# Kernel tuning notes

Hardware: AMD Instinct MI355X
Metric: run time of the kernel (lower is better)

## Reference

```python
import jax, jax.numpy as jnp
import numpy as np
import math

N_HEAD = 16
ROPE_BASE = 10000.0


def _rope(xh):
    # xh: [B, H, T, D]; rotate full head dim using half-split (GPT-NeoX style)
    B, H, T, D = xh.shape
    theta = 1.0 / (ROPE_BASE ** (jnp.arange(0, D, 2, dtype=jnp.float32) / D))  # [D/2]
    idx_theta = jnp.arange(T, dtype=jnp.float32)[:, None] * theta[None, :]      # [T, D/2]
    idx_theta2 = jnp.concatenate([idx_theta, idx_theta], axis=1)                 # [T, D]
    cos = jnp.cos(idx_theta2)[None, None]                                        # [1,1,T,D]
    sin = jnp.sin(idx_theta2)[None, None]
    d2 = D // 2
    neg_half = jnp.concatenate([-xh[..., d2:], xh[..., :d2]], axis=-1)
    return xh * cos + neg_half * sin


def setup_inputs() -> dict:
    key = jax.random.key(0)
    k1, k2, k3 = jax.random.split(key, 3)
    B, T, C = 2, 2048, 2048
    x = jax.random.normal(k1, (B, T, C), dtype=jnp.float32)
    w_attn = jax.random.normal(k2, (C, 3 * C), dtype=jnp.float32) * (1.0 / math.sqrt(C))
    w_proj = jax.random.normal(k3, (C, C), dtype=jnp.float32) * (1.0 / math.sqrt(C))
    return {"x": x, "w_attn": w_attn, "w_proj": w_proj}


def reference(x, w_attn, w_proj):
    B, T, C = x.shape
    H = N_HEAD
    D = C // H
    qkv = x @ w_attn                                   # [B,T,3C]
    q, k, v = jnp.split(qkv, 3, axis=-1)
    # [B,T,C] -> [B,H,T,D]
    to_heads = lambda t: t.reshape(B, T, H, D).transpose(0, 2, 1, 3)
    q, k, v = to_heads(q), to_heads(k), to_heads(v)
    q = _rope(q)
    k = _rope(k)
    att = jnp.einsum('bhqd,bhkd->bhqk', q, k) * (1.0 / math.sqrt(D))
    causal = jnp.tril(jnp.ones((T, T), dtype=bool))
    att = jnp.where(causal[None, None], att, -jnp.inf)
    att = jax.nn.softmax(att, axis=-1)
    y = jnp.einsum('bhqk,bhkd->bhqd', att, v)          # [B,H,T,D]
    y = y.transpose(0, 2, 1, 3).reshape(B, T, C)
    return y @ w_proj
```

## Files before the change

kernel.cpp:

```cpp
#include <hip/hip_runtime.h>
#include <hip/hip_bf16.h>
#include <math.h>

typedef __bf16 bf16;
typedef __bf16 bf16x8 __attribute__((ext_vector_type(8)));
typedef float f32x4 __attribute__((ext_vector_type(4)));
typedef float f32x16 __attribute__((ext_vector_type(16)));
typedef unsigned int u32x2 __attribute__((ext_vector_type(2)));
typedef unsigned int u32x4 __attribute__((ext_vector_type(4)));

#define MFMA16(a, b, c) __builtin_amdgcn_mfma_f32_16x16x32_bf16((a), (b), (c), 0, 0, 0)
#define MFMA32(a, b, c) __builtin_amdgcn_mfma_f32_32x32x16_bf16((a), (b), (c), 0, 0, 0)

static constexpr int Bsz = 2, Tsz = 2048, Csz = 2048, Hn = 16, Dh = 128;
static constexpr float ATTN_SCALE = 0.08838834764831845f;

__device__ __forceinline__ void gld16(const void* src, void* dst) {
    __builtin_amdgcn_global_load_lds((__attribute__((address_space(1))) void*)src,
                                     (__attribute__((address_space(3))) void*)dst,
                                     16, 0, 0);
}

__device__ __forceinline__ unsigned cvt_pk_bf16(float lo, float hi) {
    unsigned r;
    asm("v_cvt_pk_bf16_f32 %0, %1, %2" : "=v"(r) : "v"(lo), "v"(hi));
    return r;
}

__device__ __forceinline__ bf16x8 make_pfrag(float p0, float p1, float p2, float p3,
                                             float p4, float p5, float p6, float p7) {
    unsigned a0 = cvt_pk_bf16(p0, p1), a1 = cvt_pk_bf16(p2, p3);
    unsigned b0 = cvt_pk_bf16(p4, p5), b1 = cvt_pk_bf16(p6, p7);
    asm volatile("v_permlane32_swap_b32 %0, %1" : "+v"(a0), "+v"(b0));
    asm volatile("v_permlane32_swap_b32 %0, %1" : "+v"(a1), "+v"(b1));
    u32x4 w = {a0, a1, b0, b1};
    return __builtin_bit_cast(bf16x8, w);
}

__global__ __launch_bounds__(256) void cast_x_kernel(const float* __restrict__ x,
                                                     bf16* __restrict__ o, int n8) {
    int i = blockIdx.x * 256 + threadIdx.x;
    if (i >= n8) return;
    const float4* x4 = (const float4*)x;
    float4 a = x4[2 * i], b = x4[2 * i + 1];
    bf16x8 v;
    v[0] = (bf16)a.x; v[1] = (bf16)a.y; v[2] = (bf16)a.z; v[3] = (bf16)a.w;
    v[4] = (bf16)b.x; v[5] = (bf16)b.y; v[6] = (bf16)b.z; v[7] = (bf16)b.w;
    ((bf16x8*)o)[i] = v;
}

template <typename TIN>
__global__ __launch_bounds__(256) void transpose_cast_kernel(const TIN* __restrict__ in,
                                                             bf16* __restrict__ out,
                                                             int R, int Cc) {
    __shared__ float tile[64][65];
    const int tx = threadIdx.x, ty = threadIdx.y;
    in  += (size_t)blockIdx.z * R * Cc;
    out += (size_t)blockIdx.z * R * Cc;
    const int c0 = blockIdx.x * 64, r0 = blockIdx.y * 64;
#pragma unroll
    for (int j = 0; j < 16; ++j) {
        int rr = ty + j * 4;
        tile[rr][tx] = (float)in[(size_t)(r0 + rr) * Cc + c0 + tx];
    }
    __syncthreads();
#pragma unroll
    for (int j = 0; j < 16; ++j) {
        int cc = ty + j * 4;
        out[(size_t)(c0 + cc) * R + r0 + tx] = (bf16)tile[tx][cc];
    }
}

__global__ __launch_bounds__(256) void cossin_kernel(float2* __restrict__ cs) {
    int idx = blockIdx.x * 256 + threadIdx.x;
    int t = idx >> 6, i = idx & 63;
    float theta = 1.0f / powf(10000.0f, (float)(2 * i) / 128.0f);
    float ang = (float)t * theta;
    cs[idx] = make_float2(cosf(ang), sinf(ang));
}

__global__ __launch_bounds__(512, 2)
void gemm384_qkv(const bf16* __restrict__ A, const bf16* __restrict__ Bt,
                 bf16* __restrict__ Oq, bf16* __restrict__ Ok, bf16* __restrict__ Ov,
                 const float2* __restrict__ cs, int K) {
    __shared__ bf16 sA[2][128 * 64];
    __shared__ bf16 sB[2][384 * 64];
    const int tid = threadIdx.x, lane = tid & 63, wid = tid >> 6;
    const int wm = wid >> 2, wn = wid & 3;
    const int lo16 = lane & 15, hi4 = lane >> 4;

    const int cpx = gridDim.x >> 3;
    const int swz = (blockIdx.x & 7) * cpx + (blockIdx.x >> 3);
    const int by = swz & 31;
    const int bx = swz >> 5;
    const int row0 = by << 7, col0 = bx * 384;

    const int srow = tid >> 3;
    const int swzoff = (((tid & 7) ^ ((tid >> 3) & 7)) << 3);
    const bf16* srcA = A  + (size_t)(row0 + srow) * K + swzoff;
    const bf16* srcB = Bt + (size_t)(col0 + srow) * K + swzoff;
    const size_t K64 = (size_t)K * 64;
    char* const ldsA = (char*)&sA[0][0];
    char* const ldsB = (char*)&sB[0][0];
    const int wuo = wid << 10;

    auto issueA = [&](int c, int kt) {
        const bf16* s = srcA + (size_t)kt * 64;
        gld16(s,       ldsA + c * 16384 + 0    + wuo);
        gld16(s + K64, ldsA + c * 16384 + 8192 + wuo);
    };
    auto issueB = [&](int c, int kt, int u) {
        const bf16* s = srcB + (size_t)kt * 64 + (size_t)(2 * u) * K64;
        gld16(s,       ldsB + c * 49152 + u * 16384 + 0    + wuo);
        gld16(s + K64, ldsB + c * 49152 + u * 16384 + 8192 + wuo);
    };
    auto ldF = [&](const char* buf, int row, int ks) {
        return *(const bf16x8*)(buf + row * 128 + ((((ks << 2) + hi4) ^ (row & 7)) << 4));
    };

    const int arow = (wm << 6) + lo16;
    const int brow = (wn << 4) + lo16;

    f32x4 acc[4][6] = {};
    const int nkt = K >> 6;

    issueA(0, 0); issueB(0, 0, 0); issueB(0, 0, 1); issueB(0, 0, 2);
    asm volatile("s_waitcnt vmcnt(4)" ::: "memory");
    __builtin_amdgcn_s_barrier();

    for (int kt = 0; kt < nkt - 1; ++kt) {
        const int c = kt & 1;
        const char* bufA = ldsA + c * 16384;
        const char* bufB = ldsB + c * 49152;
        bf16x8 af[4][2], bq[2][2];
#pragma unroll
        for (int i = 0; i < 4; ++i) {
            af[i][0] = ldF(bufA, arow + (i << 4), 0);
            af[i][1] = ldF(bufA, arow + (i << 4), 1);
        }
#pragma unroll
        for (int j = 0; j < 2; ++j) {
            bq[j][0] = ldF(bufB, brow + (j << 6), 0);
            bq[j][1] = ldF(bufB, brow + (j << 6), 1);
        }
        issueA(c ^ 1, kt + 1); issueB(c ^ 1, kt + 1, 0); issueB(c ^ 1, kt + 1, 1);
        __builtin_amdgcn_s_barrier();
        asm volatile("s_waitcnt lgkmcnt(0)" ::: "memory");
        __builtin_amdgcn_sched_barrier(0);
        __builtin_amdgcn_s_setprio(1);
#pragma unroll
        for (int ks = 0; ks < 2; ++ks)
#pragma unroll
            for (int i = 0; i < 4; ++i)
#pragma unroll
                for (int j = 0; j < 2; ++j)
                    acc[i][j] = MFMA16(af[i][ks], bq[j][ks], acc[i][j]);
        __builtin_amdgcn_s_setprio(0);
        asm volatile("s_waitcnt vmcnt(8)" ::: "memory");
        __builtin_amdgcn_s_barrier();
#pragma unroll
        for (int j = 0; j < 2; ++j) {
            bq[j][0] = ldF(bufB, brow + ((j + 2) << 6), 0);
            bq[j][1] = ldF(bufB, brow + ((j + 2) << 6), 1);
        }
        issueB(c ^ 1, kt + 1, 2);
        __builtin_amdgcn_s_barrier();
        asm volatile("s_waitcnt lgkmcnt(0)" ::: "memory");
        __builtin_amdgcn_sched_barrier(0);
        __builtin_amdgcn_s_setprio(1);
#pragma unroll
        for (int ks = 0; ks < 2; ++ks)
#pragma unroll
            for (int i = 0; i < 4; ++i)
#pragma unroll
                for (int j = 0; j < 2; ++j)
                    acc[i][j + 2] = MFMA16(af[i][ks], bq[j][ks], acc[i][j + 2]);
        __builtin_amdgcn_s_setprio(0);
        asm volatile("s_waitcnt vmcnt(8)" ::: "memory");
        __builtin_amdgcn_s_barrier();
#pragma unroll
        for (int j = 0; j < 2; ++j) {
            bq[j][0] = ldF(bufB, brow + ((j + 4) << 6), 0);
            bq[j][1] = ldF(bufB, brow + ((j + 4) << 6), 1);
        }
        __builtin_amdgcn_s_barrier();
        asm volatile("s_waitcnt lgkmcnt(0)" ::: "memory");
        __builtin_amdgcn_sched_barrier(0);
        __builtin_amdgcn_s_setprio(1);
#pragma unroll
        for (int ks = 0; ks < 2; ++ks)
#pragma unroll
            for (int i = 0; i < 4; ++i)
#pragma unroll
                for (int j = 0; j < 2; ++j)
                    acc[i][j + 4] = MFMA16(af[i][ks], bq[j][ks], acc[i][j + 4]);
        __builtin_amdgcn_s_setprio(0);
        asm volatile("s_waitcnt vmcnt(4)" ::: "memory");
        __builtin_amdgcn_s_barrier();
    }

    {
        const int c = (nkt - 1) & 1;
        const char* bufA = ldsA + c * 16384;
        const char* bufB = ldsB + c * 49152;
        bf16x8 af[4][2], bq[2][2];
#pragma unroll
        for (int i = 0; i < 4; ++i) {
            af[i][0] = ldF(bufA, arow + (i << 4), 0);
            af[i][1] = ldF(bufA, arow + (i << 4), 1);
        }
#pragma unroll
        for (int j = 0; j < 2; ++j) {
            bq[j][0] = ldF(bufB, brow + (j << 6), 0);
            bq[j][1] = ldF(bufB, brow + (j << 6), 1);
        }
        __builtin_amdgcn_s_barrier();
        asm volatile("s_waitcnt lgkmcnt(0)" ::: "memory");
        __builtin_amdgcn_sched_barrier(0);
        __builtin_amdgcn_s_setprio(1);
#pragma unroll
        for (int ks = 0; ks < 2; ++ks)
#pragma unroll
            for (int i = 0; i < 4; ++i)
#pragma unroll
                for (int j = 0; j < 2; ++j)
                    acc[i][j] = MFMA16(af[i][ks], bq[j][ks], acc[i][j]);
        __builtin_amdgcn_s_setprio(0);
        asm volatile("s_waitcnt vmcnt(2)" ::: "memory");
        __builtin_amdgcn_s_barrier();
#pragma unroll
        for (int j = 0; j < 2; ++j) {
            bq[j][0] = ldF(bufB, brow + ((j + 2) << 6), 0);
            bq[j][1] = ldF(bufB, brow + ((j + 2) << 6), 1);
        }
        __builtin_amdgcn_s_barrier();
        asm volatile("s_waitcnt lgkmcnt(0)" ::: "memory");
        __builtin_amdgcn_sched_barrier(0);
        __builtin_amdgcn_s_setprio(1);
#pragma unroll
        for (int ks = 0; ks < 2; ++ks)
#pragma unroll
            for (int i = 0; i < 4; ++i)
#pragma unroll
                for (int j = 0; j < 2; ++j)
                    acc[i][j + 2] = MFMA16(af[i][ks], bq[j][ks], acc[i][j + 2]);
        __builtin_amdgcn_s_setprio(0);
        asm volatile("s_waitcnt vmcnt(0)" ::: "memory");
        __builtin_amdgcn_s_barrier();
#pragma unroll
        for (int j = 0; j < 2; ++j) {
            bq[j][0] = ldF(bufB, brow + ((j + 4) << 6), 0);
            bq[j][1] = ldF(bufB, brow + ((j + 4) << 6), 1);
        }
        __builtin_amdgcn_s_barrier();
        asm volatile("s_waitcnt lgkmcnt(0)" ::: "memory");
        __builtin_amdgcn_sched_barrier(0);
        __builtin_amdgcn_s_setprio(1);
#pragma unroll
        for (int ks = 0; ks < 2; ++ks)
#pragma unroll
            for (int i = 0; i < 4; ++i)
#pragma unroll
                for (int j = 0; j < 2; ++j)
                    acc[i][j + 4] = MFMA16(af[i][ks], bq[j][ks], acc[i][j + 4]);
        __builtin_amdgcn_s_setprio(0);
    }

    const int d = (wn << 4) + lo16;
#pragma unroll
    for (int p = 0; p < 3; ++p) {
        const int gcb = col0 + (p << 7);
        const int seg = gcb >> 11;
        const int hb = (gcb >> 7) & 15;
        if (seg < 2) {
            bf16* dst0 = (seg == 0) ? Oq : Ok;
            const float qs = (seg == 0) ? ATTN_SCALE : 1.0f;
#pragma unroll
            for (int mi = 0; mi < 4; ++mi)
#pragma unroll
                for (int r = 0; r < 4; ++r) {
                    const int gm = row0 + (wm << 6) + (mi << 4) + (hi4 << 2) + r;
                    const int b = gm >> 11, t = gm & 2047;
                    const float2 csv = cs[t * 64 + d];
                    bf16* drow = dst0 + ((((size_t)b * Hn + hb) * Tsz + t) << 7);
                    const float vlo = acc[mi][2 * p][r];
                    const float vhi = acc[mi][2 * p + 1][r];
                    drow[d]      = (bf16)((vlo * csv.x - vhi * csv.y) * qs);
                    drow[d + 64] = (bf16)((vhi * csv.x + vlo * csv.y) * qs);
                }
        } else {
#pragma unroll
            for (int mi = 0; mi < 4; ++mi)
#pragma unroll
                for (int r = 0; r < 4; ++r) {
                    const int gm = row0 + (wm << 6) + (mi << 4) + (hi4 << 2) + r;
                    const int b = gm >> 11, t = gm & 2047;
                    bf16* drow = Ov + ((((size_t)b * Hn + hb) * Tsz + t) << 7);
                    drow[d]      = (bf16)acc[mi][2 * p][r];
                    drow[d + 64] = (bf16)acc[mi][2 * p + 1][r];
                }
        }
    }
}

__global__ __launch_bounds__(256)
void gemm128_bt(const bf16* __restrict__ A, const bf16* __restrict__ Bt,
                float* __restrict__ Cf, int M, int N, int K) {
    __shared__ bf16 sA[128 * 64];
    __shared__ bf16 sB[128 * 64];
    const int tid = threadIdx.x;
    const int lane = tid & 63, wv = tid >> 6;
    const int wr = wv >> 1, wc = wv & 1;
    const int lo16 = lane & 15, hi4 = lane >> 4;
    const int row0 = blockIdx.y << 7, col0 = blockIdx.x << 7;

    f32x4 acc[4][4] = {};

    const int nkt = K >> 6;
    for (int kt = 0; kt < nkt; ++kt) {
        const int kbase = kt << 6;
#pragma unroll
        for (int c = 0; c < 4; ++c) {
            const int o16 = (c << 8) + tid;
            const int row = o16 >> 3, u = o16 & 7;
            const int colel = kbase + ((u ^ (row & 7)) << 3);
            gld16(A  + (size_t)(row0 + row) * K + colel,
                  (char*)sA + (((c << 8) + (wv << 6)) << 4));
            gld16(Bt + (size_t)(col0 + row) * K + colel,
                  (char*)sB + (((c << 8) + (wv << 6)) << 4));
        }
        __syncthreads();
#pragma unroll
        for (int ks = 0; ks < 2; ++ks) {
            bf16x8 af[4], bfv[4];
#pragma unroll
            for (int mi = 0; mi < 4; ++mi) {
                const int ar = (wr << 6) + (mi << 4) + lo16;
                af[mi] = *(const bf16x8*)((const char*)sA + ar * 128 +
                          (((ks << 6) + (hi4 << 4)) ^ ((ar & 7) << 4)));
            }
#pragma unroll
            for (int ni = 0; ni < 4; ++ni) {
                const int bc = (wc << 4) + (ni << 5) + lo16;
                bfv[ni] = *(const bf16x8*)((const char*)sB + bc * 128 +
                           (((ks << 6) + (hi4 << 4)) ^ ((bc & 7) << 4)));
            }
#pragma unroll
            for (int mi = 0; mi < 4; ++mi)
#pragma unroll
                for (int ni = 0; ni < 4; ++ni)
                    acc[mi][ni] = MFMA16(af[mi], bfv[ni], acc[mi][ni]);
        }
        __syncthreads();
    }

#pragma unroll
    for (int mi = 0; mi < 4; ++mi)
#pragma unroll
        for (int r = 0; r < 4; ++r) {
            const int gm = row0 + (wr << 6) + (mi << 4) + (hi4 << 2) + r;
            float* crow = Cf + (size_t)gm * N + col0 + (wc << 4) + lo16;
#pragma unroll
            for (int ni = 0; ni < 4; ++ni)
                crow[ni << 5] = acc[mi][ni][r];
        }
}

__device__ __forceinline__ void stage_tile(const bf16* __restrict__ Kb,
                                           const bf16* __restrict__ Vtb,
                                           bf16* sKc, bf16* sVc, int k0, int tid) {
#pragma unroll
    for (int c = 0; c < 4; ++c) {
        const int off = (c << 12) + (tid << 4);
        const int row = off >> 8, u = (off >> 4) & 15;
        gld16(Kb + (size_t)(k0 + row) * Dh + ((u ^ (row & 7)) << 3), (char*)sKc + off);
        const int dv = off >> 7, uv = (off >> 4) & 7;
        gld16(Vtb + (size_t)dv * Tsz + k0 + ((uv ^ (dv & 7)) << 3), (char*)sVc + off);
    }
}

__global__ __launch_bounds__(256, 2)
void attn_kernel(const bf16* __restrict__ Q, const bf16* __restrict__ K,
                 const bf16* __restrict__ Vt, bf16* __restrict__ Y) {
    __shared__ bf16 sK[2][64 * 128];
    __shared__ bf16 sV[2][128 * 64];
    const int tid = threadIdx.x, lane = tid & 63, wv = tid >> 6;
    const int lo32 = lane & 31, hl = lane >> 5;

    const int i = blockIdx.x;
    const int g = i >> 5;
    const int bh = i & 31;
    const int t = (i < 256) ? (15 - g) : (g - 8);
    const int b = bh >> 4, h = bh & 15;

    const int q0 = t << 7;
    const int q0w = q0 + (wv << 5);
    const int qg = q0w + lo32;

    const bf16* Kb  = K  + (size_t)bh * (Tsz * Dh);
    const bf16* Vtb = Vt + (size_t)bh * (Tsz * Dh);
    const bf16* Qp  = Q  + (size_t)bh * (Tsz * Dh) + (size_t)qg * Dh;

    bf16x8 qf[8];
#pragma unroll
    for (int kc = 0; kc < 8; ++kc)
        qf[kc] = *(const bf16x8*)(Qp + (kc << 4) + (hl << 3));

    float m = -1e30f, lsum = 0.f;
    f32x16 o[4] = {};

    const int nt_block = 2 * t + 2;
    const int nt_warp = ((q0w + 31) >> 6) + 1;

    stage_tile(Kb, Vtb, &sK[0][0], &sV[0][0], 0, tid);

    int cur = 0;
    for (int kt = 0; kt < nt_block; ++kt) {
        __syncthreads();
        if (kt + 1 < nt_block)
            stage_tile(Kb, Vtb, &sK[cur ^ 1][0], &sV[cur ^ 1][0], (kt + 1) << 6, tid);
        if (kt < nt_warp) {
            const int k0 = kt << 6;
            const bf16* kbuf = &sK[cur][0];
            const bf16* vbuf = &sV[cur][0];
            f32x16 s0 = {}, s1 = {};
            const int swk = lo32 & 7;
            __builtin_amdgcn_s_setprio(1);
#pragma unroll
            for (int kc = 0; kc < 8; ++kc) {
                bf16x8 kf0 = *(const bf16x8*)((const char*)kbuf + lo32 * 256 +
                              ((((kc << 1) + hl) ^ swk) << 4));
                s0 = MFMA32(kf0, qf[kc], s0);
                bf16x8 kf1 = *(const bf16x8*)((const char*)kbuf + (32 + lo32) * 256 +
                              ((((kc << 1) + hl) ^ swk) << 4));
                s1 = MFMA32(kf1, qf[kc], s1);
            }
            __builtin_amdgcn_s_setprio(0);

            const bool bnd = (k0 + 63 > q0w);
            if (bnd) {
#pragma unroll
                for (int r = 0; r < 16; ++r) {
                    const int kl = (r & 3) + ((r >> 2) << 3) + (hl << 2);
                    if (k0 + kl > qg)      s0[r] = -1e30f;
                    if (k0 + 32 + kl > qg) s1[r] = -1e30f;
                }
            }
            float pm = s0[0];
#pragma unroll
            for (int r = 1; r < 16; ++r) pm = fmaxf(pm, s0[r]);
#pragma unroll
            for (int r = 0; r < 16; ++r) pm = fmaxf(pm, s1[r]);
            pm = fmaxf(pm, __shfl_xor(pm, 32));

            if (__any(pm > m + 8.0f)) {
                const float mn = fmaxf(m, pm);
                const float sc = __expf(m - mn);
                m = mn;
                lsum *= sc;
#pragma unroll
                for (int db = 0; db < 4; ++db)
#pragma unroll
                    for (int r = 0; r < 16; ++r) o[db][r] *= sc;
            }
            float rs = 0.f;
            if (bnd) {
#pragma unroll
                for (int r = 0; r < 16; ++r) {
                    float e0 = (s0[r] > -1e29f) ? __expf(s0[r] - m) : 0.f;
                    float e1 = (s1[r] > -1e29f) ? __expf(s1[r] - m) : 0.f;
                    s0[r] = e0; s1[r] = e1; rs += e0 + e1;
                }
            } else {
#pragma unroll
                for (int r = 0; r < 16; ++r) {
                    float e0 = __expf(s0[r] - m);
                    float e1 = __expf(s1[r] - m);
                    s0[r] = e0; s1[r] = e1; rs += e0 + e1;
                }
            }
            rs += __shfl_xor(rs, 32);
            lsum += rs;

            bf16x8 pb0 = make_pfrag(s0[0], s0[1], s0[2],  s0[3],  s0[4],  s0[5],  s0[6],  s0[7]);
            bf16x8 pb1 = make_pfrag(s0[8], s0[9], s0[10], s0[11], s0[12], s0[13], s0[14], s0[15]);
            bf16x8 pb2 = make_pfrag(s1[0], s1[1], s1[2],  s1[3],  s1[4],  s1[5],  s1[6],  s1[7]);
            bf16x8 pb3 = make_pfrag(s1[8], s1[9], s1[10], s1[11], s1[12], s1[13], s1[14], s1[15]);

            __builtin_amdgcn_s_setprio(1);
#pragma unroll
            for (int db = 0; db < 4; ++db) {
                const int rd = (db << 5) + lo32;
                const char* vrow = (const char*)vbuf + rd * 128;
                const int sw = rd & 7;
                bf16x8 v0 = *(const bf16x8*)(vrow + (((0 + hl) ^ sw) << 4));
                o[db] = MFMA32(v0, pb0, o[db]);
                bf16x8 v1 = *(const bf16x8*)(vrow + (((2 + hl) ^ sw) << 4));
                o[db] = MFMA32(v1, pb1, o[db]);
                bf16x8 v2 = *(const bf16x8*)(vrow + (((4 + hl) ^ sw) << 4));
                o[db] = MFMA32(v2, pb2, o[db]);
                bf16x8 v3 = *(const bf16x8*)(vrow + (((6 + hl) ^ sw) << 4));
                o[db] = MFMA32(v3, pb3, o[db]);
            }
            __builtin_amdgcn_s_setprio(0);
        }
        cur ^= 1;
    }

    const float inv = 1.0f / lsum;
    const size_t rowoff = ((size_t)b * Tsz + qg) * (size_t)Csz + (size_t)h * 128;
#pragma unroll
    for (int db = 0; db < 4; ++db)
#pragma unroll
        for (int gg = 0; gg < 4; ++gg) {
            unsigned w0 = cvt_pk_bf16(o[db][4 * gg + 0] * inv, o[db][4 * gg + 1] * inv);
            unsigned w1 = cvt_pk_bf16(o[db][4 * gg + 2] * inv, o[db][4 * gg + 3] * inv);
            u32x2 w = {w0, w1};
            *(u32x2*)(Y + rowoff + (db << 5) + (gg << 3) + (hl << 2)) = w;
        }
}

extern "C" void kernel_launch(void* const* d_in, const int* in_sizes, int n_in,
                              void* d_out, int out_size, void* d_ws, size_t ws_size,
                              hipStream_t stream) {
    const float* x      = (const float*)d_in[0];
    const float* w_attn = (const float*)d_in[1];
    const float* w_proj = (const float*)d_in[2];
    float* out = (float*)d_out;

    char* ws = (char*)d_ws;
    bf16* Xb  = (bf16*)(ws);
    bf16* Wat = (bf16*)(ws + 16777216);
    bf16* Wpt = (bf16*)(ws + 41943040);
    bf16* Qr  = (bf16*)(ws + 50331648);
    bf16* Kr  = (bf16*)(ws + 67108864);
    bf16* Vb  = (bf16*)(ws + 83886080);
    bf16* Vt  = (bf16*)(ws + 100663296);
    bf16* Yb  = (bf16*)(ws + 117440512);
    float2* cs = (float2*)(ws + 134217728);

    cast_x_kernel<<<4096, 256, 0, stream>>>(x, Xb, (Bsz * Tsz * Csz) / 8);
    transpose_cast_kernel<float><<<dim3(96, 32, 1), dim3(64, 4), 0, stream>>>(w_attn, Wat, 2048, 6144);
    transpose_cast_kernel<float><<<dim3(32, 32, 1), dim3(64, 4), 0, stream>>>(w_proj, Wpt, 2048, 2048);
    cossin_kernel<<<512, 256, 0, stream>>>(cs);

    gemm384_qkv<<<512, 512, 0, stream>>>(Xb, Wat, Qr, Kr, Vb, cs, 2048);
    transpose_cast_kernel<bf16><<<dim3(2, 32, 32), dim3(64, 4), 0, stream>>>(Vb, Vt, 2048, 128);

    attn_kernel<<<dim3(512), 256, 0, stream>>>(Qr, Kr, Vt, Yb);

    gemm128_bt<<<dim3(16, 32), 256, 0, stream>>>(Yb, Wpt, out, 4096, 2048, 2048);
}
```

Measured before the change: 241.5 us.

## Replace output projection GEMM with double-buffered 128x256 pipelined kernel

Replaces the simple 128x128 single-buffered projection GEMM with a 512-thread 128x256 tile kernel. It double-buffers LDS, splits each K step into two half-phases so global-to-LDS loads overlap the MFMA work, raises wave priority around the MFMA blocks and remaps block indices for L2 locality. The aim is to hide load latency and cut barrier stalls in the final GEMM. It relies on hand-set vmcnt counts and fixed N=2048 / 32 row-blocks, which makes it fragile if shapes change.

```diff
diff --git a/kernel.cpp b/kernel.cpp
--- a/kernel.cpp
+++ b/kernel.cpp
@@ -303,66 +303,119 @@
     }
 }
 
-__global__ __launch_bounds__(256)
-void gemm128_bt(const bf16* __restrict__ A, const bf16* __restrict__ Bt,
-                float* __restrict__ Cf, int M, int N, int K) {
-    __shared__ bf16 sA[128 * 64];
-    __shared__ bf16 sB[128 * 64];
-    const int tid = threadIdx.x;
-    const int lane = tid & 63, wv = tid >> 6;
-    const int wr = wv >> 1, wc = wv & 1;
+__global__ __launch_bounds__(512, 2)
+void gemm256_proj(const bf16* __restrict__ A, const bf16* __restrict__ Bt,
+                  float* __restrict__ Cf, int K) {
+    __shared__ bf16 sA[2][128 * 64];
+    __shared__ bf16 sB[2][256 * 64];
+    const int tid = threadIdx.x, lane = tid & 63, wid = tid >> 6;
+    const int wm = wid >> 2, wn = wid & 3;
     const int lo16 = lane & 15, hi4 = lane >> 4;
-    const int row0 = blockIdx.y << 7, col0 = blockIdx.x << 7;
+    const int N = 2048;
+
+    const int cpx = gridDim.x >> 3;
+    const int swz = (blockIdx.x & 7) * cpx + (blockIdx.x >> 3);
+    const int by = swz & 31;
+    const int bx = swz >> 5;
+    const int row0 = by << 7, col0 = bx << 8;
+
+    const int srow = tid >> 3;
+    const int swzoff = (((tid & 7) ^ ((tid >> 3) & 7)) << 3);
+    const bf16* srcA = A  + (size_t)(row0 + srow) * K + swzoff;
+    const bf16* srcB = Bt + (size_t)(col0 + srow) * K + swzoff;
+    const size_t K64 = (size_t)K * 64;
+    char* const ldsA = (char*)&sA[0][0];
+    char* const ldsB = (char*)&sB[0][0];
+    const int wuo = wid << 10;
+
+    auto issueA = [&](int c, int kt) {
+        const bf16* s = srcA + (size_t)kt * 64;
+        gld16(s,       ldsA + c * 16384 + 0    + wuo);
+        gld16(s + K64, ldsA + c * 16384 + 8192 + wuo);
+    };
+    auto issueB = [&](int c, int kt, int u) {
+        const bf16* s = srcB + (size_t)kt * 64 + (size_t)(2 * u) * K64;
+        gld16(s,       ldsB + c * 32768 + u * 16384 + 0    + wuo);
+        gld16(s + K64, ldsB + c * 32768 + u * 16384 + 8192 + wuo);
+    };
+    auto ldF = [&](const char* buf, int row, int ks) {
+        return *(const bf16x8*)(buf + row * 128 + ((((ks << 2) + hi4) ^ (row & 7)) << 4));
+    };
+
+    const int arow = (wm << 6) + lo16;
+    const int brow = (wn << 4) + lo16;
 
     f32x4 acc[4][4] = {};
-
     const int nkt = K >> 6;
+
+    issueA(0, 0); issueB(0, 0, 0); issueB(0, 0, 1);
+    if (nkt > 1) { issueA(1, 1); issueB(1, 1, 0); }
+    asm volatile("s_waitcnt vmcnt(4)" ::: "memory");
+    __builtin_amdgcn_s_barrier();
+
     for (int kt = 0; kt < nkt; ++kt) {
-        const int kbase = kt << 6;
-#pragma unroll
-        for (int c = 0; c < 4; ++c) {
-            const int o16 = (c << 8) + tid;
-            const int row = o16 >> 3, u = o16 & 7;
-            const int colel = kbase + ((u ^ (row & 7)) << 3);
-            gld16(A  + (size_t)(row0 + row) * K + colel,
-                  (char*)sA + (((c << 8) + (wv << 6)) << 4));
-            gld16(Bt + (size_t)(col0 + row) * K + colel,
-                  (char*)sB + (((c << 8) + (wv << 6)) << 4));
-        }
-        __syncthreads();
-#pragma unroll
-        for (int ks = 0; ks < 2; ++ks) {
-            bf16x8 af[4], bfv[4];
-#pragma unroll
-            for (int mi = 0; mi < 4; ++mi) {
-                const int ar = (wr << 6) + (mi << 4) + lo16;
-                af[mi] = *(const bf16x8*)((const char*)sA + ar * 128 +
-                          (((ks << 6) + (hi4 << 4)) ^ ((ar & 7) << 4)));
-            }
-#pragma unroll
-            for (int ni = 0; ni < 4; ++ni) {
-                const int bc = (wc << 4) + (ni << 5) + lo16;
-                bfv[ni] = *(const bf16x8*)((const char*)sB + bc * 128 +
-                           (((ks << 6) + (hi4 << 4)) ^ ((bc & 7) << 4)));
-            }
-#pragma unroll
-            for (int mi = 0; mi < 4; ++mi)
-#pragma unroll
-                for (int ni = 0; ni < 4; ++ni)
-                    acc[mi][ni] = MFMA16(af[mi], bfv[ni], acc[mi][ni]);
-        }
-        __syncthreads();
+        const int c = kt & 1;
+        const char* bufA = ldsA + c * 16384;
+        const char* bufB = ldsB + c * 32768;
+        bf16x8 af[4][2], bq[2][2];
+#pragma unroll
+        for (int i = 0; i < 4; ++i) {
+            af[i][0] = ldF(bufA, arow + (i << 4), 0);
+            af[i][1] = ldF(bufA, arow + (i << 4), 1);
+        }
+#pragma unroll
+        for (int j = 0; j < 2; ++j) {
+            bq[j][0] = ldF(bufB, brow + (j << 6), 0);
+            bq[j][1] = ldF(bufB, brow + (j << 6), 1);
+        }
+        if (kt + 1 < nkt) issueB(c ^ 1, kt + 1, 1);
+        __builtin_amdgcn_s_barrier();
+        asm volatile("s_waitcnt lgkmcnt(0)" ::: "memory");
+        __builtin_amdgcn_sched_barrier(0);
+        __builtin_amdgcn_s_setprio(1);
+#pragma unroll
+        for (int ks = 0; ks < 2; ++ks)
+#pragma unroll
+            for (int i = 0; i < 4; ++i)
+#pragma unroll
+                for (int j = 0; j < 2; ++j)
+                    acc[i][j] = MFMA16(af[i][ks], bq[j][ks], acc[i][j]);
+        __builtin_amdgcn_s_setprio(0);
+        if (kt + 1 < nkt) asm volatile("s_waitcnt vmcnt(6)" ::: "memory");
+        else              asm volatile("s_waitcnt vmcnt(0)" ::: "memory");
+        __builtin_amdgcn_s_barrier();
+#pragma unroll
+        for (int j = 0; j < 2; ++j) {
+            bq[j][0] = ldF(bufB, brow + ((j + 2) << 6), 0);
+            bq[j][1] = ldF(bufB, brow + ((j + 2) << 6), 1);
+        }
+        if (kt + 2 < nkt) { issueA(c, kt + 2); issueB(c, kt + 2, 0); }
+        __builtin_amdgcn_s_barrier();
+        asm volatile("s_waitcnt lgkmcnt(0)" ::: "memory");
+        __builtin_amdgcn_sched_barrier(0);
+        __builtin_amdgcn_s_setprio(1);
+#pragma unroll
+        for (int ks = 0; ks < 2; ++ks)
+#pragma unroll
+            for (int i = 0; i < 4; ++i)
+#pragma unroll
+                for (int j = 0; j < 2; ++j)
+                    acc[i][j + 2] = MFMA16(af[i][ks], bq[j][ks], acc[i][j + 2]);
+        __builtin_amdgcn_s_setprio(0);
+        if (kt + 2 < nkt)      asm volatile("s_waitcnt vmcnt(6)" ::: "memory");
+        else if (kt + 1 < nkt) asm volatile("s_waitcnt vmcnt(2)" ::: "memory");
+        __builtin_amdgcn_s_barrier();
     }
 
 #pragma unroll
     for (int mi = 0; mi < 4; ++mi)
 #pragma unroll
         for (int r = 0; r < 4; ++r) {
-            const int gm = row0 + (wr << 6) + (mi << 4) + (hi4 << 2) + r;
-            float* crow = Cf + (size_t)gm * N + col0 + (wc << 4) + lo16;
-#pragma unroll
-            for (int ni = 0; ni < 4; ++ni)
-                crow[ni << 5] = acc[mi][ni][r];
+            const int gm = row0 + (wm << 6) + (mi << 4) + (hi4 << 2) + r;
+            float* crow = Cf + (size_t)gm * N + col0 + (wn << 4) + lo16;
+#pragma unroll
+            for (int nj = 0; nj < 4; ++nj)
+                crow[nj << 6] = acc[mi][nj][r];
         }
 }
 
@@ -549,5 +602,5 @@
 
     attn_kernel<<<dim3(512), 256, 0, stream>>>(Qr, Kr, Vt, Yb);
 
-    gemm128_bt<<<dim3(16, 32), 256, 0, stream>>>(Yb, Wpt, out, 4096, 2048, 2048);
-}
+    gemm256_proj<<<256, 512, 0, stream>>>(Yb, Wpt, out, 2048);
+}
```

Measured after the change: 239.6 us. No clear change (-0.8%).
